# Kernel tuning notes

Hardware: AMD Instinct MI355X
Metric: run time of the kernel (lower is better)

## Reference

```python
import jax, jax.numpy as jnp
import numpy as np

B = 4096      # batch of users
D = 128       # embedding_dim
NA = 128      # num_anchors
AD = 128      # anchor_dim
NU = 100000   # num_users
NI = 50000    # num_items


def setup_inputs() -> dict:
    key = jax.random.key(0)
    ks = jax.random.split(key, 10)
    s = 0.05
    return {
        "user_indices": jax.random.randint(ks[0], (B,), 0, NU),
        "pos_item_indices": jax.random.randint(ks[1], (B,), 0, NI),
        "user_table": jax.random.normal(ks[2], (NU, D), dtype=jnp.float32) * s,
        "item_table": jax.random.normal(ks[3], (NI, D), dtype=jnp.float32) * s,
        "ln1_g": jnp.ones((D,), jnp.float32),
        "ln1_b": jnp.zeros((D,), jnp.float32),
        "send_W": jax.random.normal(ks[4], (D, AD), dtype=jnp.float32) * s,
        "send_a": jax.random.normal(ks[5], (2 * AD,), dtype=jnp.float32) * s,
        "anchors": jax.random.normal(ks[6], (NA, AD), dtype=jnp.float32) * s,
        "ln2_g": jnp.ones((NA,), jnp.float32),
        "ln2_b": jnp.zeros((NA,), jnp.float32),
        "recv_W": jax.random.normal(ks[7], (NA, D), dtype=jnp.float32) * s,
        "recv_a": jax.random.normal(ks[8], (2 * D,), dtype=jnp.float32) * s,
    }


def _layernorm(x, g, b, eps=1e-5):
    m = jnp.mean(x, axis=-1, keepdims=True)
    v = jnp.mean((x - m) ** 2, axis=-1, keepdims=True)
    return (x - m) * jax.lax.rsqrt(v + eps) * g + b


def _fca(x, W, a):
    # FullyConnectedAttention: score[i,j] = [t_i ; t_j] . a = t_i.a1 + t_j.a2
    # (decomposed form of the torch repeat/cat -> same math, no [B,B,2F] tensor)
    t = x @ W                       # [B, F]
    f = t.shape[-1]
    a1, a2 = a[:f], a[f:]
    e = (t @ a1)[:, None] + (t @ a2)[None, :]   # [B, B]
    w = jax.nn.softmax(e, axis=1)
    return w @ t                    # [B, F]


def reference(user_indices, pos_item_indices, user_table, item_table,
              ln1_g, ln1_b, send_W, send_a, anchors, ln2_g, ln2_b,
              recv_W, recv_a):
    u = user_table[user_indices]                 # [B, D]
    # AdaptiveAnchorConvolution
    nf = _layernorm(u, ln1_g, ln1_b)             # feature_norm
    sent = _fca(nf, send_W, send_a)              # send_attention -> [B, AD]
    ap = sent @ anchors.T                        # anchor projection [B, NA]
    na = _layernorm(ap, ln2_g, ln2_b)            # anchor_norm
    rec = _fca(na, recv_W, recv_a)               # receive_attention -> [B, D]
    ue = u + jnp.sin(rec)                        # residual + sin
    pos = item_table[pos_item_indices]           # [B, D]
    preds = ue @ item_table.T                    # [B, NI]
    return preds, ue, pos
```

## Files before the change

### kernel.cpp

```cpp
#include <hip/hip_runtime.h>
#include <hip/hip_bf16.h>

#define BB   4096
#define DD   128
#define NII  50000

typedef __attribute__((ext_vector_type(8))) short  bf8_t;
typedef __attribute__((ext_vector_type(4))) float  f4_t;
typedef __attribute__((ext_vector_type(4))) unsigned short us4_t;
typedef __attribute__((ext_vector_type(4))) float  fl4_t;

static __device__ __forceinline__ unsigned short f2bf(float f) {
    unsigned u = __float_as_uint(f);
    u += 0x7fffu + ((u >> 16) & 1u);
    return (unsigned short)(u >> 16);
}

static __device__ __forceinline__ void gload_lds16(const void* g, void* lds) {
    __builtin_amdgcn_global_load_lds(
        (const __attribute__((address_space(1))) void*)g,
        (__attribute__((address_space(3))) void*)lds, 16, 0, 0);
}

__global__ __launch_bounds__(128) void k1_embed_send(
    const int* __restrict__ uidx, const float* __restrict__ utab,
    const float* __restrict__ g1, const float* __restrict__ b1,
    const float* __restrict__ sendW, const float* __restrict__ senda,
    float* __restrict__ t_out, float* __restrict__ s2_out)
{
    __shared__ float sb[128];
    __shared__ float nf[128];
    const int row = blockIdx.x;
    const int tid = threadIdx.x;
    const long urow = uidx[row];
    const float x = utab[urow * 128 + tid];

    sb[tid] = x; __syncthreads();
    for (int s = 64; s > 0; s >>= 1) { if (tid < s) sb[tid] += sb[tid + s]; __syncthreads(); }
    const float mean = sb[0] * (1.0f / 128.0f); __syncthreads();
    const float dv = x - mean;
    sb[tid] = dv * dv; __syncthreads();
    for (int s = 64; s > 0; s >>= 1) { if (tid < s) sb[tid] += sb[tid + s]; __syncthreads(); }
    const float var = sb[0] * (1.0f / 128.0f);
    const float rs = rsqrtf(var + 1e-5f);
    nf[tid] = dv * rs * g1[tid] + b1[tid];
    __syncthreads();

    float acc = 0.f;
    #pragma unroll 8
    for (int d = 0; d < 128; ++d) acc += nf[d] * sendW[d * 128 + tid];
    t_out[row * 128 + tid] = acc;

    const float p = acc * senda[128 + tid];
    __syncthreads();
    sb[tid] = p; __syncthreads();
    for (int s = 64; s > 0; s >>= 1) { if (tid < s) sb[tid] += sb[tid + s]; __syncthreads(); }
    if (tid == 0) s2_out[row] = sb[0];
}

__global__ __launch_bounds__(256) void k2b_colsum(
    const float* __restrict__ t, const float* __restrict__ s2,
    float* __restrict__ partial)
{
    __shared__ float ew[128];
    __shared__ float sb[256];
    const int tid = threadIdx.x;

    float m = -1e30f;
    for (int i = tid; i < BB; i += 256) m = fmaxf(m, s2[i]);
    sb[tid] = m; __syncthreads();
    for (int s = 128; s > 0; s >>= 1) { if (tid < s) sb[tid] = fmaxf(sb[tid], sb[tid + s]); __syncthreads(); }
    m = sb[0]; __syncthreads();

    const int rbase = blockIdx.x * 128;
    if (tid < 128) ew[tid] = __expf(s2[rbase + tid] - m);
    __syncthreads();
    const int col = tid & 127, half = tid >> 7;
    float acc = 0.f;
    for (int j = half; j < 128; j += 2)
        acc += ew[j] * t[(rbase + j) * 128 + col];
    sb[tid] = acc; __syncthreads();
    if (tid < 128) partial[blockIdx.x * 128 + tid] = sb[tid] + sb[tid + 128];
}

__global__ __launch_bounds__(128) void k2c_finish(
    const float* __restrict__ partial, const float* __restrict__ s2,
    const float* __restrict__ anchors, const float* __restrict__ g2,
    const float* __restrict__ b2, const float* __restrict__ recvW,
    float* __restrict__ r_out)
{
    __shared__ float sent[128];
    __shared__ float na_s[128];
    __shared__ float sb[128];
    const int tid = threadIdx.x;

    float m = -1e30f;
    for (int i = tid; i < BB; i += 128) m = fmaxf(m, s2[i]);
    sb[tid] = m; __syncthreads();
    for (int s = 64; s > 0; s >>= 1) { if (tid < s) sb[tid] = fmaxf(sb[tid], sb[tid + s]); __syncthreads(); }
    m = sb[0]; __syncthreads();
    float sum = 0.f;
    for (int i = tid; i < BB; i += 128) sum += __expf(s2[i] - m);
    sb[tid] = sum; __syncthreads();
    for (int s = 64; s > 0; s >>= 1) { if (tid < s) sb[tid] += sb[tid + s]; __syncthreads(); }
    const float S = sb[0]; __syncthreads();

    float acc = 0.f;
    for (int b = 0; b < 32; ++b) acc += partial[b * 128 + tid];
    sent[tid] = acc / S;
    __syncthreads();
    float ap = 0.f;
    for (int c = 0; c < 128; ++c) ap += sent[c] * anchors[tid * 128 + c];
    sb[tid] = ap; __syncthreads();
    for (int s = 64; s > 0; s >>= 1) { if (tid < s) sb[tid] += sb[tid + s]; __syncthreads(); }
    const float mean = sb[0] * (1.0f / 128.0f); __syncthreads();
    const float dv = ap - mean;
    sb[tid] = dv * dv; __syncthreads();
    for (int s = 64; s > 0; s >>= 1) { if (tid < s) sb[tid] += sb[tid + s]; __syncthreads(); }
    const float var = sb[0] * (1.0f / 128.0f);
    const float rs = rsqrtf(var + 1e-5f);
    na_s[tid] = dv * rs * g2[tid] + b2[tid];
    __syncthreads();
    float t2 = 0.f;
    for (int k = 0; k < 128; ++k) t2 += na_s[k] * recvW[k * 128 + tid];
    r_out[tid] = sinf(t2);
}

__global__ __launch_bounds__(256) void k3_ue_pos(
    const int* __restrict__ uidx, const float* __restrict__ utab,
    const int* __restrict__ pidx, const float* __restrict__ itab,
    const float* __restrict__ r, float* __restrict__ ue_out,
    float* __restrict__ pos_out, unsigned short* __restrict__ uebf)
{
    const int gid = blockIdx.x * 256 + threadIdx.x;
    const int i = gid >> 7, d = gid & 127;
    const float rv = r[d];
    const float u = utab[(long)uidx[i] * 128 + d];
    const float ue = u + rv;
    ue_out[gid] = ue;
    uebf[gid] = f2bf(ue);
    pos_out[gid] = itab[(long)pidx[i] * 128 + d];
}

__global__ __launch_bounds__(256) void k3b_cvt_item(
    const float* __restrict__ itab, unsigned short* __restrict__ ibf)
{
    const int gid = blockIdx.x * 256 + threadIdx.x;
    const fl4_t v = *(const fl4_t*)(itab + (long)gid * 4);
    us4_t o;
    o.x = f2bf(v.x); o.y = f2bf(v.y); o.z = f2bf(v.z); o.w = f2bf(v.w);
    *(us4_t*)(ibf + (long)gid * 4) = o;
}

__global__ __launch_bounds__(256, 3) void k4_gemm(
    const unsigned short* __restrict__ uebf,
    const unsigned short* __restrict__ ibf,
    float* __restrict__ preds)
{
    __shared__ unsigned short lA[128 * 128];
    __shared__ unsigned short lB[64 * 128];

    const int tid = threadIdx.x;
    const int wave = tid >> 6, lane = tid & 63;
    const int l15 = lane & 15, kg = lane >> 4;
    const int col0 = blockIdx.x * 64;
    const int row0 = blockIdx.y * 128;

    #pragma unroll
    for (int i = 0; i < 8; ++i) {
        const int o   = (i * 256 + tid) * 16;
        const int r   = o >> 8;
        const int ch  = (o >> 4) & 15;
        const int sw  = ch ^ (r & 15);
        gload_lds16(uebf + (size_t)(row0 + r) * 128 + sw * 8,
                    (char*)lA + i * 4096 + wave * 1024);
    }
    #pragma unroll
    for (int i = 0; i < 4; ++i) {
        const int o   = (i * 256 + tid) * 16;
        const int r   = o >> 8;
        const int ch  = (o >> 4) & 15;
        const int sw  = ch ^ (r & 15);
        const int bc  = (col0 + r) < NII ? (col0 + r) : (NII - 1);
        gload_lds16(ibf + (size_t)bc * 128 + sw * 8,
                    (char*)lB + i * 4096 + wave * 1024);
    }

    const int wr = wave >> 1, wc = wave & 1;

    f4_t acc[4][2];
    #pragma unroll
    for (int m = 0; m < 4; ++m)
        #pragma unroll
        for (int n = 0; n < 2; ++n) acc[m][n] = (f4_t){0.f, 0.f, 0.f, 0.f};

    __syncthreads();

    #pragma unroll
    for (int kk = 0; kk < 4; ++kk) {
        const int c = kk * 4 + kg;
        bf8_t a[4], b[2];
        #pragma unroll
        for (int m = 0; m < 4; ++m) {
            const int r = wr * 64 + m * 16 + l15;
            a[m] = *(const bf8_t*)((const char*)lA + r * 256 + (c ^ (r & 15)) * 16);
        }
        #pragma unroll
        for (int n = 0; n < 2; ++n) {
            const int r = wc * 32 + n * 16 + l15;
            b[n] = *(const bf8_t*)((const char*)lB + r * 256 + (c ^ (r & 15)) * 16);
        }
        #pragma unroll
        for (int m = 0; m < 4; ++m)
            #pragma unroll
            for (int n = 0; n < 2; ++n)
                acc[m][n] = __builtin_amdgcn_mfma_f32_16x16x32_bf16(b[n], a[m], acc[m][n], 0, 0, 0);
    }

    #pragma unroll
    for (int m = 0; m < 4; ++m) {
        const long grow = row0 + wr * 64 + m * 16 + l15;
        #pragma unroll
        for (int n = 0; n < 2; ++n) {
            const int gcol = col0 + wc * 32 + n * 16 + kg * 4;
            if (gcol < NII)
                *(fl4_t*)(preds + grow * NII + gcol) = acc[m][n];
        }
    }
}

extern "C" void kernel_launch(void* const* d_in, const int* in_sizes, int n_in,
                              void* d_out, int out_size, void* d_ws, size_t ws_size,
                              hipStream_t stream) {
    const int*   uidx   = (const int*)  d_in[0];
    const int*   pidx   = (const int*)  d_in[1];
    const float* utab   = (const float*)d_in[2];
    const float* itab   = (const float*)d_in[3];
    const float* g1     = (const float*)d_in[4];
    const float* b1     = (const float*)d_in[5];
    const float* sendW  = (const float*)d_in[6];
    const float* senda  = (const float*)d_in[7];
    const float* anchors= (const float*)d_in[8];
    const float* g2     = (const float*)d_in[9];
    const float* b2     = (const float*)d_in[10];
    const float* recvW  = (const float*)d_in[11];

    char* ws = (char*)d_ws;
    float* t_ws    = (float*)(ws + 0);
    float* s2_ws   = (float*)(ws + 2097152);
    float* part_ws = (float*)(ws + 2113600);
    float* r_ws    = (float*)(ws + 2129984);
    unsigned short* uebf = (unsigned short*)(ws + 2130496);
    unsigned short* ibf  = (unsigned short*)(ws + 3179072);

    float* preds   = (float*)d_out;
    float* ue_out  = preds + (long)BB * NII;
    float* pos_out = ue_out + BB * DD;

    k3b_cvt_item<<<6250, 256, 0, stream>>>(itab, ibf);
    k1_embed_send<<<4096, 128, 0, stream>>>(uidx, utab, g1, b1, sendW, senda, t_ws, s2_ws);
    k2b_colsum<<<32, 256, 0, stream>>>(t_ws, s2_ws, part_ws);
    k2c_finish<<<1, 128, 0, stream>>>(part_ws, s2_ws, anchors, g2, b2, recvW, r_ws);
    k3_ue_pos<<<2048, 256, 0, stream>>>(uidx, utab, pidx, itab, r_ws, ue_out, pos_out, uebf);
    k4_gemm<<<dim3(782, 32, 1), 256, 0, stream>>>(uebf, ibf, preds);
}
```

Baseline: 260.7 us.

## Make item GEMM persistent over column tiles with double-buffered B loads

```diff
diff --git a/kernel.cpp b/kernel.cpp
--- a/kernel.cpp
+++ b/kernel.cpp
@@ -4,6 +4,8 @@
 #define BB   4096
 #define DD   128
 #define NII  50000
+#define NT4  782
+#define CPC  49
 
 typedef __attribute__((ext_vector_type(8))) short  bf8_t;
 typedef __attribute__((ext_vector_type(4))) float  f4_t;
@@ -152,80 +154,102 @@
     *(us4_t*)(ibf + (long)gid * 4) = o;
 }
 
-__global__ __launch_bounds__(256, 3) void k4_gemm(
+__global__ __launch_bounds__(256, 2) void k4_gemm(
     const unsigned short* __restrict__ uebf,
     const unsigned short* __restrict__ ibf,
     float* __restrict__ preds)
 {
     __shared__ unsigned short lA[128 * 128];
-    __shared__ unsigned short lB[64 * 128];
+    __shared__ unsigned short lB0[64 * 128];
+    __shared__ unsigned short lB1[64 * 128];
 
     const int tid = threadIdx.x;
     const int wave = tid >> 6, lane = tid & 63;
     const int l15 = lane & 15, kg = lane >> 4;
-    const int col0 = blockIdx.x * 64;
-    const int row0 = blockIdx.y * 128;
+    const int chunk = blockIdx.x;
+    const int mstripe = blockIdx.y;
+    const int base = chunk * CPC;
+    const int ns = min(CPC, NT4 - base);
+    const int row0 = mstripe * 128;
 
     #pragma unroll
     for (int i = 0; i < 8; ++i) {
-        const int o   = (i * 256 + tid) * 16;
-        const int r   = o >> 8;
-        const int ch  = (o >> 4) & 15;
-        const int sw  = ch ^ (r & 15);
+        const int o = (i * 256 + tid) * 16, r = o >> 8, ch = (o >> 4) & 15, sw = ch ^ (r & 15);
         gload_lds16(uebf + (size_t)(row0 + r) * 128 + sw * 8,
                     (char*)lA + i * 4096 + wave * 1024);
     }
-    #pragma unroll
-    for (int i = 0; i < 4; ++i) {
-        const int o   = (i * 256 + tid) * 16;
-        const int r   = o >> 8;
-        const int ch  = (o >> 4) & 15;
-        const int sw  = ch ^ (r & 15);
-        const int bc  = (col0 + r) < NII ? (col0 + r) : (NII - 1);
-        gload_lds16(ibf + (size_t)bc * 128 + sw * 8,
-                    (char*)lB + i * 4096 + wave * 1024);
+    {
+        const int c0 = base * 64;
+        #pragma unroll
+        for (int i = 0; i < 4; ++i) {
+            const int o = (i * 256 + tid) * 16, r = o >> 8, ch = (o >> 4) & 15, sw = ch ^ (r & 15);
+            const int bc = (c0 + r) < NII ? (c0 + r) : (NII - 1);
+            gload_lds16(ibf + (size_t)bc * 128 + sw * 8,
+                        (char*)lB0 + i * 4096 + wave * 1024);
+        }
     }
+    asm volatile("s_waitcnt vmcnt(0)" ::: "memory");
+    __builtin_amdgcn_sched_barrier(0);
+    __builtin_amdgcn_s_barrier();
 
     const int wr = wave >> 1, wc = wave & 1;
 
-    f4_t acc[4][2];
-    #pragma unroll
-    for (int m = 0; m < 4; ++m)
-        #pragma unroll
-        for (int n = 0; n < 2; ++n) acc[m][n] = (f4_t){0.f, 0.f, 0.f, 0.f};
-
-    __syncthreads();
-
-    #pragma unroll
-    for (int kk = 0; kk < 4; ++kk) {
-        const int c = kk * 4 + kg;
-        bf8_t a[4], b[2];
+    for (int j = 0; j < ns; ++j) {
+        if (j + 1 < ns) {
+            const int c0n = (base + j + 1) * 64;
+            char* dst = (char*)((j & 1) ? lB0 : lB1);
+            #pragma unroll
+            for (int i = 0; i < 4; ++i) {
+                const int o = (i * 256 + tid) * 16, r = o >> 8, ch = (o >> 4) & 15, sw = ch ^ (r & 15);
+                const int bc = (c0n + r) < NII ? (c0n + r) : (NII - 1);
+                gload_lds16(ibf + (size_t)bc * 128 + sw * 8, dst + i * 4096 + wave * 1024);
+            }
+        }
+
+        const unsigned short* bb = (j & 1) ? lB1 : lB0;
+
+        f4_t acc[4][2];
+        #pragma unroll
+        for (int m = 0; m < 4; ++m)
+            #pragma unroll
+            for (int n = 0; n < 2; ++n) acc[m][n] = (f4_t){0.f, 0.f, 0.f, 0.f};
+
+        #pragma unroll
+        for (int kk = 0; kk < 4; ++kk) {
+            const int c = kk * 4 + kg;
+            bf8_t a[4], b[2];
+            #pragma unroll
+            for (int m = 0; m < 4; ++m) {
+                const int r = wr * 64 + m * 16 + l15;
+                a[m] = *(const bf8_t*)((const char*)lA + r * 256 + (c ^ (r & 15)) * 16);
+            }
+            #pragma unroll
+            for (int n = 0; n < 2; ++n) {
+                const int r = wc * 32 + n * 16 + l15;
+                b[n] = *(const bf8_t*)((const char*)bb + r * 256 + (c ^ (r & 15)) * 16);
+            }
+            #pragma unroll
+            for (int m = 0; m < 4; ++m)
+                #pragma unroll
+                for (int n = 0; n < 2; ++n)
+                    acc[m][n] = __builtin_amdgcn_mfma_f32_16x16x32_bf16(b[n], a[m], acc[m][n], 0, 0, 0);
+        }
+
+        const int col0 = (base + j) * 64;
         #pragma unroll
         for (int m = 0; m < 4; ++m) {
-            const int r = wr * 64 + m * 16 + l15;
-            a[m] = *(const bf8_t*)((const char*)lA + r * 256 + (c ^ (r & 15)) * 16);
-        }
-        #pragma unroll
-        for (int n = 0; n < 2; ++n) {
-            const int r = wc * 32 + n * 16 + l15;
-            b[n] = *(const bf8_t*)((const char*)lB + r * 256 + (c ^ (r & 15)) * 16);
-        }
-        #pragma unroll
-        for (int m = 0; m < 4; ++m)
-            #pragma unroll
-            for (int n = 0; n < 2; ++n)
-                acc[m][n] = __builtin_amdgcn_mfma_f32_16x16x32_bf16(b[n], a[m], acc[m][n], 0, 0, 0);
-    }
-
-    #pragma unroll
-    for (int m = 0; m < 4; ++m) {
-        const long grow = row0 + wr * 64 + m * 16 + l15;
-        #pragma unroll
-        for (int n = 0; n < 2; ++n) {
-            const int gcol = col0 + wc * 32 + n * 16 + kg * 4;
-            if (gcol < NII)
-                *(fl4_t*)(preds + grow * NII + gcol) = acc[m][n];
-        }
+            const long grow = row0 + wr * 64 + m * 16 + l15;
+            #pragma unroll
+            for (int n = 0; n < 2; ++n) {
+                const int gcol = col0 + wc * 32 + n * 16 + kg * 4;
+                if (gcol < NII)
+                    *(fl4_t*)(preds + grow * NII + gcol) = acc[m][n];
+            }
+        }
+
+        asm volatile("s_waitcnt vmcnt(8)" ::: "memory");
+        __builtin_amdgcn_sched_barrier(0);
+        __builtin_amdgcn_s_barrier();
     }
 }
 
@@ -262,5 +286,5 @@
     k2b_colsum<<<32, 256, 0, stream>>>(t_ws, s2_ws, part_ws);
     k2c_finish<<<1, 128, 0, stream>>>(part_ws, s2_ws, anchors, g2, b2, recvW, r_ws);
     k3_ue_pos<<<2048, 256, 0, stream>>>(uidx, utab, pidx, itab, r_ws, ue_out, pos_out, uebf);
-    k4_gemm<<<dim3(782, 32, 1), 256, 0, stream>>>(uebf, ibf, preds);
-}
+    k4_gemm<<<dim3(16, 32, 1), 256, 0, stream>>>(uebf, ibf, preds);
+}
```

After: 319.1 us. 1.22x slower.
